# Kernel optimization log

Hardware: AMD Instinct MI355X
Metric: run time of the kernel (lower is better)

The kernel has to match this reference:

```python
import jax, jax.numpy as jnp
from jax import lax
import numpy as np

B, T, I, H, O = 256, 1024, 64, 25, 64

def setup_inputs() -> dict:
    key = jax.random.key(0)
    ks = jax.random.split(key, 7)
    s_ih = 1.0 / np.sqrt(H)  # PyTorch LSTM init scale (uniform +-1/sqrt(H))
    return {
        "x": jax.random.normal(ks[0], (B, T, I), dtype=jnp.float32),
        "W_ih": jax.random.uniform(ks[1], (4 * H, I), minval=-s_ih, maxval=s_ih, dtype=jnp.float32),
        "W_hh": jax.random.uniform(ks[2], (4 * H, H), minval=-s_ih, maxval=s_ih, dtype=jnp.float32),
        "b_ih": jax.random.uniform(ks[3], (4 * H,), minval=-s_ih, maxval=s_ih, dtype=jnp.float32),
        "b_hh": jax.random.uniform(ks[4], (4 * H,), minval=-s_ih, maxval=s_ih, dtype=jnp.float32),
        "W_fc": jax.random.uniform(ks[5], (O, H), minval=-s_ih, maxval=s_ih, dtype=jnp.float32),
        "b_fc": jax.random.uniform(ks[6], (O,), minval=-s_ih, maxval=s_ih, dtype=jnp.float32),
    }

def reference(x, W_ih, W_hh, b_ih, b_hh, W_fc, b_fc):
    # x: [B, T, I]; PyTorch LSTM gate order: i, f, g, o
    Bh = x.shape[0]
    Hh = W_hh.shape[1]
    # Precompute the input contribution to all gates for all timesteps (one big GEMM).
    gates_x = jnp.einsum('bti,gi->btg', x, W_ih) + b_ih + b_hh  # [B, T, 4H]

    def step(carry, gx):
        h, c = carry
        g = gx + h @ W_hh.T                     # [B, 4H]
        i, f, gg, o = jnp.split(g, 4, axis=-1)
        i = jax.nn.sigmoid(i)
        f = jax.nn.sigmoid(f)
        gg = jnp.tanh(gg)
        o = jax.nn.sigmoid(o)
        c = f * c + i * gg
        h = o * jnp.tanh(c)
        return (h, c), h

    h0 = jnp.zeros((Bh, Hh), dtype=x.dtype)
    c0 = jnp.zeros((Bh, Hh), dtype=x.dtype)
    _, hs = lax.scan(step, (h0, c0), jnp.swapaxes(gates_x, 0, 1))  # hs: [T, B, H]
    hs = jnp.swapaxes(hs, 0, 1)                                   # [B, T, H]
    return hs @ W_fc.T + b_fc                                     # [B, T, O]
```

## Files before the change

kernel.cpp:

```cpp
#include <hip/hip_runtime.h>
#include <hip/hip_fp16.h>


#define Bn 256
#define Tn 1024
#define In 64
#define Hn 25
#define Gn 100
#define On 64

#define SCL_S -1.44269504089f
#define SCL_T -2.88539008178f

typedef __attribute__((ext_vector_type(8))) short short8;
typedef __attribute__((ext_vector_type(4))) float f32x4;
typedef __attribute__((ext_vector_type(4))) int i32x4;

__device__ __forceinline__ float frcp(float x) { return __builtin_amdgcn_rcpf(x); }
__device__ __forceinline__ float ex2(float x) {
    float r;
    asm("v_exp_f32 %0, %1\n\ts_nop 1" : "=v"(r) : "v"(x));
    return r;
}
__device__ __forceinline__ float bcast(float v, int lane) {
    return __int_as_float(__builtin_amdgcn_readlane(__float_as_int(v), lane));
}
__device__ __forceinline__ float xswap(float x) {
    float a = x, b = x;
    asm("s_nop 0\n\tv_permlane32_swap_b32 %0, %1\n\ts_nop 0"
        : "+v"(a), "+v"(b));
    return b;
}
__device__ __forceinline__ unsigned short f2bf(float f) {
    unsigned u = __float_as_uint(f);
    return (unsigned short)((u + 0x7FFFu + ((u >> 16) & 1u)) >> 16);
}

__device__ __forceinline__ void colmap(int n, int& g, float& scl) {
    if (n < 50) {
        const int r = n >> 1;
        g = ((n & 1) ? 2 : 0) * Hn + r;
        scl = (n & 1) ? SCL_T : SCL_S;
    } else {
        const int m = n - 50, r = m >> 1;
        g = ((m & 1) ? 3 : 1) * Hn + r;
        scl = SCL_S;
    }
}

__global__ __launch_bounds__(192, 1)
void lstm_fused(const float* __restrict__ x, const float* __restrict__ W_ih,
                const float* __restrict__ W_hh, const float* __restrict__ b_ih,
                const float* __restrict__ b_hh, const float* __restrict__ W_fc,
                const float* __restrict__ b_fc, float* __restrict__ out) {
    __shared__ short lB[112 * 72];
    __shared__ float lbias[112];
    __shared__ short xlds[16 * 72];
    __shared__ float gbuf[2][800];
    __shared__ float hbuf[16][64];

    const int tid  = threadIdx.x;
    const int wid  = tid >> 6;
    const int lane = tid & 63;
    const int b    = blockIdx.x;

    for (int i = tid; i < 112 * 64; i += 192) {
        const int n = i >> 6, k = i & 63;
        float v = 0.f;
        if (n < Gn) {
            int g; float scl;
            colmap(n, g, scl);
            v = W_ih[(size_t)g * In + k] * scl;
        }
        lB[n * 72 + k] = (short)f2bf(v);
    }
    if (tid < 112) {
        float v = 0.f;
        if (tid < Gn) {
            int g; float scl;
            colmap(tid, g, scl);
            v = (b_ih[g] + b_hh[g]) * scl;
        }
        lbias[tid] = v;
    }
    for (int i = tid; i < 16 * 72; i += 192) xlds[i] = 0;
    __syncthreads();

    float wAv[25], wBv[25];
    float c = 0.f, h = 0.f;
    float sB = 1.f, dB = 0.f;
    int coff = 0;
    float wFC[25];
    float bfc = 0.f;
    float* op = nullptr;
    short8 bf0[7], bf1[7];
    float biasv[7];
    float4 xra, xrb;
    const float* xb = x + (size_t)b * Tn * In;

    const int quad = lane >> 4;
    const int l16  = lane & 15;

    if (wid == 0) {
        const bool lo = lane < 32;
        const int rr  = min(lane & 31, Hn - 1);
        const float sclA = SCL_S;
        const float sclB = lo ? SCL_T : SCL_S;
        sB = lo ? 2.f : 1.f;
        dB = lo ? -1.f : 0.f;
        const float* rowA = W_hh + (size_t)((lo ? 0 : 1) * Hn + rr) * Hn;
        const float* rowB = W_hh + (size_t)((lo ? 2 : 3) * Hn + rr) * Hn;
#pragma unroll
        for (int j = 0; j < 25; ++j) {
            wAv[j] = rowA[j] * sclA;
            wBv[j] = rowB[j] * sclB;
        }
        coff = 2 * rr + (lo ? 0 : 50);
    } else if (wid == 1) {
#pragma unroll
        for (int j = 0; j < 25; ++j) wFC[j] = W_fc[(size_t)lane * Hn + j];
        bfc = b_fc[lane];
        op = out + (size_t)b * Tn * On + lane;
    } else {
#pragma unroll
        for (int nt = 0; nt < 7; ++nt) {
            const int col = nt * 16 + l16;
            bf0[nt] = *(const short8*)&lB[col * 72 + 0  + quad * 8];
            bf1[nt] = *(const short8*)&lB[col * 72 + 32 + quad * 8];
            biasv[nt] = lbias[col];
        }
        {
            const float4 a = *(const float4*)(xb + lane * 8);
            const float4 d = *(const float4*)(xb + lane * 8 + 4);
            i32x4 p;
            p.x = (int)(((unsigned)f2bf(a.y) << 16) | f2bf(a.x));
            p.y = (int)(((unsigned)f2bf(a.w) << 16) | f2bf(a.z));
            p.z = (int)(((unsigned)f2bf(d.y) << 16) | f2bf(d.x));
            p.w = (int)(((unsigned)f2bf(d.w) << 16) | f2bf(d.z));
            *(i32x4*)&xlds[(lane >> 3) * 72 + (lane & 7) * 8] = p;
        }
    }
    __syncthreads();

    if (wid == 2) {
        const short8 a0 = *(const short8*)&xlds[l16 * 72 + 0  + quad * 8];
        const short8 a1 = *(const short8*)&xlds[l16 * 72 + 32 + quad * 8];
#pragma unroll
        for (int nt = 0; nt < 7; ++nt) {
            f32x4 acc = {biasv[nt], biasv[nt], biasv[nt], biasv[nt]};
            acc = __builtin_amdgcn_mfma_f32_16x16x32_bf16(a0, bf0[nt], acc, 0, 0, 0);
            acc = __builtin_amdgcn_mfma_f32_16x16x32_bf16(a1, bf1[nt], acc, 0, 0, 0);
            const int col = nt * 16 + l16;
            if (lane < 32 && col < Gn) {
#pragma unroll
                for (int i = 0; i < 4; ++i)
                    gbuf[0][(quad * 4 + i) * 100 + col] = acc[i];
            }
        }
        xra = *(const float4*)(xb + 512 + lane * 8);
        xrb = *(const float4*)(xb + 512 + lane * 8 + 4);
    }
    __syncthreads();

#pragma unroll 1
    for (int k = 0; k < 129; ++k) {
        if (wid == 0) {
            if (k < 128) {
                const int kb = k & 1;
                float2 g[8];
#pragma unroll
                for (int s = 0; s < 8; ++s)
                    g[s] = *(const float2*)&gbuf[kb][s * 100 + coff];
#pragma unroll
                for (int s = 0; s < 8; ++s) {
                    const int t = k * 8 + s;
                    float aA0 = g[s].x, aB0 = g[s].y;
                    float aA1 = 0.f,   aB1 = 0.f;
#pragma unroll
                    for (int j = 0; j < 24; j += 2) {
                        const float h0 = bcast(h, j);
                        const float h1 = bcast(h, j + 1);
                        aA0 = fmaf(wAv[j],     h0, aA0);
                        aB0 = fmaf(wBv[j],     h0, aB0);
                        aA1 = fmaf(wAv[j + 1], h1, aA1);
                        aB1 = fmaf(wBv[j + 1], h1, aB1);
                    }
                    {
                        const float h0 = bcast(h, 24);
                        aA0 = fmaf(wAv[24], h0, aA0);
                        aB0 = fmaf(wBv[24], h0, aB0);
                    }
                    const float aA = aA0 + aA1;
                    const float aB = aB0 + aB1;

                    const float actA = frcp(1.f + ex2(aA));
                    const float actB = sB * frcp(1.f + ex2(aB)) + dB;
                    const float Fg = xswap(actA);
                    const float Og = xswap(actB);
                    c = Fg * c + actA * actB;
                    const float th = 2.f * frcp(1.f + ex2(c * SCL_T)) - 1.f;
                    h = Og * th;

                    hbuf[t & 15][lane] = h;
                }
            }
        } else if (wid == 1) {
            if (k >= 1) {
#pragma unroll
                for (int s = 0; s < 8; ++s) {
                    const int t = (k - 1) * 8 + s;
                    const int sl = t & 15;
                    float a0 = bfc, a1 = 0.f;
#pragma unroll
                    for (int j = 0; j < 24; j += 2) {
                        a0 = fmaf(hbuf[sl][j],     wFC[j],     a0);
                        a1 = fmaf(hbuf[sl][j + 1], wFC[j + 1], a1);
                    }
                    a0 = fmaf(hbuf[sl][24], wFC[24], a0);
                    op[(size_t)t * On] = a0 + a1;
                }
            }
        } else {
            if (k < 127) {
                i32x4 p;
                p.x = (int)(((unsigned)f2bf(xra.y) << 16) | f2bf(xra.x));
                p.y = (int)(((unsigned)f2bf(xra.w) << 16) | f2bf(xra.z));
                p.z = (int)(((unsigned)f2bf(xrb.y) << 16) | f2bf(xrb.x));
                p.w = (int)(((unsigned)f2bf(xrb.w) << 16) | f2bf(xrb.z));
                *(i32x4*)&xlds[(lane >> 3) * 72 + (lane & 7) * 8] = p;
                if (k < 126) {
                    const float* xs = xb + (size_t)(k + 2) * 512;
                    xra = *(const float4*)(xs + lane * 8);
                    xrb = *(const float4*)(xs + lane * 8 + 4);
                }
                asm volatile("s_waitcnt lgkmcnt(0)" ::: "memory");
                const short8 a0 = *(const short8*)&xlds[l16 * 72 + 0  + quad * 8];
                const short8 a1 = *(const short8*)&xlds[l16 * 72 + 32 + quad * 8];
                const int nb = (k + 1) & 1;
#pragma unroll
                for (int nt = 0; nt < 7; ++nt) {
                    f32x4 acc = {biasv[nt], biasv[nt], biasv[nt], biasv[nt]};
                    acc = __builtin_amdgcn_mfma_f32_16x16x32_bf16(a0, bf0[nt], acc, 0, 0, 0);
                    acc = __builtin_amdgcn_mfma_f32_16x16x32_bf16(a1, bf1[nt], acc, 0, 0, 0);
                    const int col = nt * 16 + l16;
                    if (lane < 32 && col < Gn) {
#pragma unroll
                        for (int i = 0; i < 4; ++i)
                            gbuf[nb][(quad * 4 + i) * 100 + col] = acc[i];
                    }
                }
            }
        }
        asm volatile("s_waitcnt lgkmcnt(0)" ::: "memory");
        __builtin_amdgcn_s_barrier();
        asm volatile("" ::: "memory");
    }
}

extern "C" void kernel_launch(void* const* d_in, const int* in_sizes, int n_in,
                              void* d_out, int out_size, void* d_ws, size_t ws_size,
                              hipStream_t stream) {
    const float* x    = (const float*)d_in[0];
    const float* W_ih = (const float*)d_in[1];
    const float* W_hh = (const float*)d_in[2];
    const float* b_ih = (const float*)d_in[3];
    const float* b_hh = (const float*)d_in[4];
    const float* W_fc = (const float*)d_in[5];
    const float* b_fc = (const float*)d_in[6];
    float* out = (float*)d_out;

    lstm_fused<<<Bn, 192, 0, stream>>>(x, W_ih, W_hh, b_ih, b_hh,
                                       W_fc, b_fc, out);
}
```

Measured before the change: 310.5 us.

## Double chunk size to 16 timesteps per barrier and widen recurrence ILP

Each pipeline chunk now covers 16 timesteps instead of 8. The input-projection wave uses the full 16 rows of its MFMA tile, and the gate and hidden-state buffers grow to match. This halves the number of block-wide barriers across the recurrent loop. The recurrent dot product is split into four partial accumulators, and the activation math is folded into FMAs to shorten the serial dependency chain. In exchange the kernel uses more LDS and registers, and each chunk is longer, so pipeline fill and drain cost more.

Measured after the change: 319.2 us. +2.8%, slower.

```diff
diff --git a/kernel.cpp b/kernel.cpp
--- a/kernel.cpp
+++ b/kernel.cpp
@@ -8,6 +8,8 @@
 #define Hn 25
 #define Gn 100
 #define On 64
+#define CH 16
+#define NCH (Tn / CH)
 
 #define SCL_S -1.44269504089f
 #define SCL_T -2.88539008178f
@@ -34,6 +36,9 @@
 __device__ __forceinline__ unsigned short f2bf(float f) {
     unsigned u = __float_as_uint(f);
     return (unsigned short)((u + 0x7FFFu + ((u >> 16) & 1u)) >> 16);
+}
+__device__ __forceinline__ int pk2(float lo, float hi) {
+    return (int)(((unsigned)f2bf(hi) << 16) | f2bf(lo));
 }
 
 __device__ __forceinline__ void colmap(int n, int& g, float& scl) {
@@ -56,8 +61,8 @@
     __shared__ short lB[112 * 72];
     __shared__ float lbias[112];
     __shared__ short xlds[16 * 72];
-    __shared__ float gbuf[2][800];
-    __shared__ float hbuf[16][64];
+    __shared__ float gbuf[2][CH * 100];
+    __shared__ float hbuf[32][64];
 
     const int tid  = threadIdx.x;
     const int wid  = tid >> 6;
@@ -83,7 +88,6 @@
         }
         lbias[tid] = v;
     }
-    for (int i = tid; i < 16 * 72; i += 192) xlds[i] = 0;
     __syncthreads();
 
     float wAv[25], wBv[25];
@@ -95,7 +99,7 @@
     float* op = nullptr;
     short8 bf0[7], bf1[7];
     float biasv[7];
-    float4 xra, xrb;
+    float4 xr0, xr1, xr2, xr3;
     const float* xb = x + (size_t)b * Tn * In;
 
     const int quad = lane >> 4;
@@ -129,16 +133,18 @@
             bf1[nt] = *(const short8*)&lB[col * 72 + 32 + quad * 8];
             biasv[nt] = lbias[col];
         }
-        {
-            const float4 a = *(const float4*)(xb + lane * 8);
-            const float4 d = *(const float4*)(xb + lane * 8 + 4);
-            i32x4 p;
-            p.x = (int)(((unsigned)f2bf(a.y) << 16) | f2bf(a.x));
-            p.y = (int)(((unsigned)f2bf(a.w) << 16) | f2bf(a.z));
-            p.z = (int)(((unsigned)f2bf(d.y) << 16) | f2bf(d.x));
-            p.w = (int)(((unsigned)f2bf(d.w) << 16) | f2bf(d.z));
-            *(i32x4*)&xlds[(lane >> 3) * 72 + (lane & 7) * 8] = p;
-        }
+        const int row = lane >> 2, cb = (lane & 3) * 16;
+        const float4 a = *(const float4*)(xb + lane * 16 + 0);
+        const float4 d = *(const float4*)(xb + lane * 16 + 4);
+        const float4 e = *(const float4*)(xb + lane * 16 + 8);
+        const float4 f = *(const float4*)(xb + lane * 16 + 12);
+        i32x4 p0, p1;
+        p0.x = pk2(a.x, a.y); p0.y = pk2(a.z, a.w);
+        p0.z = pk2(d.x, d.y); p0.w = pk2(d.z, d.w);
+        p1.x = pk2(e.x, e.y); p1.y = pk2(e.z, e.w);
+        p1.z = pk2(f.x, f.y); p1.w = pk2(f.z, f.w);
+        *(i32x4*)&xlds[row * 72 + cb + 0] = p0;
+        *(i32x4*)&xlds[row * 72 + cb + 8] = p1;
     }
     __syncthreads();
 
@@ -151,65 +157,74 @@
             acc = __builtin_amdgcn_mfma_f32_16x16x32_bf16(a0, bf0[nt], acc, 0, 0, 0);
             acc = __builtin_amdgcn_mfma_f32_16x16x32_bf16(a1, bf1[nt], acc, 0, 0, 0);
             const int col = nt * 16 + l16;
-            if (lane < 32 && col < Gn) {
+            if (col < Gn) {
 #pragma unroll
                 for (int i = 0; i < 4; ++i)
                     gbuf[0][(quad * 4 + i) * 100 + col] = acc[i];
             }
         }
-        xra = *(const float4*)(xb + 512 + lane * 8);
-        xrb = *(const float4*)(xb + 512 + lane * 8 + 4);
+        const float* xs = xb + 1024;
+        xr0 = *(const float4*)(xs + lane * 16 + 0);
+        xr1 = *(const float4*)(xs + lane * 16 + 4);
+        xr2 = *(const float4*)(xs + lane * 16 + 8);
+        xr3 = *(const float4*)(xs + lane * 16 + 12);
     }
     __syncthreads();
 
 #pragma unroll 1
-    for (int k = 0; k < 129; ++k) {
+    for (int k = 0; k <= NCH; ++k) {
         if (wid == 0) {
-            if (k < 128) {
+            if (k < NCH) {
                 const int kb = k & 1;
-                float2 g[8];
-#pragma unroll
-                for (int s = 0; s < 8; ++s)
+                float2 g[CH];
+#pragma unroll
+                for (int s = 0; s < CH; ++s)
                     g[s] = *(const float2*)&gbuf[kb][s * 100 + coff];
 #pragma unroll
-                for (int s = 0; s < 8; ++s) {
-                    const int t = k * 8 + s;
-                    float aA0 = g[s].x, aB0 = g[s].y;
-                    float aA1 = 0.f,   aB1 = 0.f;
-#pragma unroll
-                    for (int j = 0; j < 24; j += 2) {
+                for (int s = 0; s < CH; ++s) {
+                    float aA0 = g[s].x, aA1 = 0.f, aA2 = 0.f, aA3 = 0.f;
+                    float aB0 = g[s].y, aB1 = 0.f, aB2 = 0.f, aB3 = 0.f;
+#pragma unroll
+                    for (int j = 0; j < 24; j += 4) {
                         const float h0 = bcast(h, j);
                         const float h1 = bcast(h, j + 1);
+                        const float h2 = bcast(h, j + 2);
+                        const float h3 = bcast(h, j + 3);
                         aA0 = fmaf(wAv[j],     h0, aA0);
                         aB0 = fmaf(wBv[j],     h0, aB0);
                         aA1 = fmaf(wAv[j + 1], h1, aA1);
                         aB1 = fmaf(wBv[j + 1], h1, aB1);
+                        aA2 = fmaf(wAv[j + 2], h2, aA2);
+                        aB2 = fmaf(wBv[j + 2], h2, aB2);
+                        aA3 = fmaf(wAv[j + 3], h3, aA3);
+                        aB3 = fmaf(wBv[j + 3], h3, aB3);
                     }
                     {
                         const float h0 = bcast(h, 24);
                         aA0 = fmaf(wAv[24], h0, aA0);
                         aB0 = fmaf(wBv[24], h0, aB0);
                     }
-                    const float aA = aA0 + aA1;
-                    const float aB = aB0 + aB1;
-
-                    const float actA = frcp(1.f + ex2(aA));
-                    const float actB = sB * frcp(1.f + ex2(aB)) + dB;
-                    const float Fg = xswap(actA);
-                    const float Og = xswap(actB);
-                    c = Fg * c + actA * actB;
-                    const float th = 2.f * frcp(1.f + ex2(c * SCL_T)) - 1.f;
-                    h = Og * th;
-
-                    hbuf[t & 15][lane] = h;
+                    const float aA = (aA0 + aA1) + (aA2 + aA3);
+                    const float aB = (aB0 + aB1) + (aB2 + aB3);
+
+                    const float rA = frcp(1.f + ex2(aA));
+                    const float rB = frcp(1.f + ex2(aB));
+                    const float Fg = xswap(rA);
+                    const float Og = xswap(rB);
+                    const float actB = fmaf(sB, rB, dB);
+                    c = fmaf(Fg, c, rA * actB);
+                    const float r2 = frcp(1.f + ex2(c * SCL_T));
+                    h = fmaf(Og + Og, r2, -Og);
+
+                    hbuf[(k * CH + s) & 31][lane] = h;
                 }
             }
         } else if (wid == 1) {
             if (k >= 1) {
 #pragma unroll
-                for (int s = 0; s < 8; ++s) {
-                    const int t = (k - 1) * 8 + s;
-                    const int sl = t & 15;
+                for (int s = 0; s < CH; ++s) {
+                    const int t = (k - 1) * CH + s;
+                    const int sl = t & 31;
                     float a0 = bfc, a1 = 0.f;
 #pragma unroll
                     for (int j = 0; j < 24; j += 2) {
@@ -221,17 +236,21 @@
                 }
             }
         } else {
-            if (k < 127) {
-                i32x4 p;
-                p.x = (int)(((unsigned)f2bf(xra.y) << 16) | f2bf(xra.x));
-                p.y = (int)(((unsigned)f2bf(xra.w) << 16) | f2bf(xra.z));
-                p.z = (int)(((unsigned)f2bf(xrb.y) << 16) | f2bf(xrb.x));
-                p.w = (int)(((unsigned)f2bf(xrb.w) << 16) | f2bf(xrb.z));
-                *(i32x4*)&xlds[(lane >> 3) * 72 + (lane & 7) * 8] = p;
-                if (k < 126) {
-                    const float* xs = xb + (size_t)(k + 2) * 512;
-                    xra = *(const float4*)(xs + lane * 8);
-                    xrb = *(const float4*)(xs + lane * 8 + 4);
+            if (k < NCH - 1) {
+                const int row = lane >> 2, cb = (lane & 3) * 16;
+                i32x4 p0, p1;
+                p0.x = pk2(xr0.x, xr0.y); p0.y = pk2(xr0.z, xr0.w);
+                p0.z = pk2(xr1.x, xr1.y); p0.w = pk2(xr1.z, xr1.w);
+                p1.x = pk2(xr2.x, xr2.y); p1.y = pk2(xr2.z, xr2.w);
+                p1.z = pk2(xr3.x, xr3.y); p1.w = pk2(xr3.z, xr3.w);
+                *(i32x4*)&xlds[row * 72 + cb + 0] = p0;
+                *(i32x4*)&xlds[row * 72 + cb + 8] = p1;
+                if (k < NCH - 2) {
+                    const float* xs = xb + (size_t)(k + 2) * (CH * In);
+                    xr0 = *(const float4*)(xs + lane * 16 + 0);
+                    xr1 = *(const float4*)(xs + lane * 16 + 4);
+                    xr2 = *(const float4*)(xs + lane * 16 + 8);
+                    xr3 = *(const float4*)(xs + lane * 16 + 12);
                 }
                 asm volatile("s_waitcnt lgkmcnt(0)" ::: "memory");
                 const short8 a0 = *(const short8*)&xlds[l16 * 72 + 0  + quad * 8];
@@ -243,7 +262,7 @@
                     acc = __builtin_amdgcn_mfma_f32_16x16x32_bf16(a0, bf0[nt], acc, 0, 0, 0);
                     acc = __builtin_amdgcn_mfma_f32_16x16x32_bf16(a1, bf1[nt], acc, 0, 0, 0);
                     const int col = nt * 16 + l16;
-                    if (lane < 32 && col < Gn) {
+                    if (col < Gn) {
 #pragma unroll
                         for (int i = 0; i < 4; ++i)
                             gbuf[nb][(quad * 4 + i) * 100 + col] = acc[i];
```
